# Optimization experiments

Measured on AMD Instinct MI355X. Metric: run time of the kernel, lower is better.

## Reference

```python
import jax, jax.numpy as jnp
import numpy as np

L, S, N, E, H = 1024, 1024, 4, 1024, 16


def setup_inputs() -> dict:
    key = jax.random.key(0)
    ks = jax.random.split(key, 7)
    return {
        "query": jax.random.normal(ks[0], (L, N, E), jnp.float32),
        "key": jax.random.normal(ks[1], (S, N, E), jnp.float32),
        "value": jax.random.normal(ks[2], (S, N, E), jnp.float32),
        "in_proj_weight": jax.random.normal(ks[3], (3 * E, E), jnp.float32) * (E ** -0.5),
        "in_proj_bias": jax.random.normal(ks[4], (3 * E,), jnp.float32) * 0.02,
        "out_proj_weight": jax.random.normal(ks[5], (E, E), jnp.float32) * (E ** -0.5),
        "out_proj_bias": jax.random.normal(ks[6], (E,), jnp.float32) * 0.02,
        "num_heads": H,
    }


def _split_heads(x, n, h, hd):
    # (T, N, E) -> (N*h, T, hd), matching torch view(T, N*h, hd).transpose(0, 1)
    t = x.shape[0]
    return jnp.transpose(x.reshape(t, n * h, hd), (1, 0, 2))


def reference(query, key, value, in_proj_weight, in_proj_bias,
              out_proj_weight, out_proj_bias, num_heads):
    tgt_len, bsz, embed_dim = query.shape
    src_len = key.shape[0]
    head_dim = embed_dim // num_heads
    scaling = float(head_dim) ** -0.5

    # packed QKV projection (torch F.linear: x @ W.T + b), sliced as in source
    q = query @ in_proj_weight[:embed_dim].T + in_proj_bias[:embed_dim]
    k = key @ in_proj_weight[embed_dim:2 * embed_dim].T + in_proj_bias[embed_dim:2 * embed_dim]
    v = value @ in_proj_weight[2 * embed_dim:].T + in_proj_bias[2 * embed_dim:]
    q = q * scaling

    q = _split_heads(q, bsz, num_heads, head_dim)  # (N*H, L, hd)
    k = _split_heads(k, bsz, num_heads, head_dim)  # (N*H, S, hd)
    v = _split_heads(v, bsz, num_heads, head_dim)  # (N*H, S, hd)

    scores = jnp.einsum('bld,bsd->bls', q, k)           # (N*H, L, S)
    attn = jax.nn.softmax(scores, axis=-1)
    ctx = jnp.einsum('bls,bsd->bld', attn, v)           # (N*H, L, hd)

    # (N*H, L, hd) -> (L, N, E)
    ctx = jnp.transpose(ctx, (1, 0, 2)).reshape(tgt_len, bsz, embed_dim)
    attn_output = ctx @ out_proj_weight.T + out_proj_bias

    # need_weights=True path: average over heads -> (N, L, S)
    attn_weights = attn.reshape(bsz, num_heads, tgt_len, src_len).sum(axis=1) / num_heads
    return attn_output, attn_weights
```

## Files before the change

### kernel.cpp

```cpp
#include <hip/hip_runtime.h>

typedef unsigned short u16;
typedef __attribute__((ext_vector_type(8))) short short8;
typedef __attribute__((ext_vector_type(4))) float f32x4;

__device__ __forceinline__ u16 f2bf(float f) {
  unsigned int i = __float_as_uint(f);
  i += 0x7fffu + ((i >> 16) & 1u);
  return (u16)(i >> 16);
}

__device__ __forceinline__ short8 cvt8(const float* p) {
  float4 a = ((const float4*)p)[0];
  float4 b = ((const float4*)p)[1];
  short8 r;
  r[0] = (short)f2bf(a.x); r[1] = (short)f2bf(a.y);
  r[2] = (short)f2bf(a.z); r[3] = (short)f2bf(a.w);
  r[4] = (short)f2bf(b.x); r[5] = (short)f2bf(b.y);
  r[6] = (short)f2bf(b.z); r[7] = (short)f2bf(b.w);
  return r;
}

__global__ __launch_bounds__(256) void convert_bf16(
    const float* __restrict__ q, const float* __restrict__ k,
    const float* __restrict__ v, const float* __restrict__ Wi,
    const float* __restrict__ Wo,
    u16* __restrict__ qb, u16* __restrict__ kb, u16* __restrict__ vb,
    u16* __restrict__ Wib, u16* __restrict__ Wob)
{
  const float* src; u16* dst; int len8;
  switch (blockIdx.y) {
    case 0:  src = q;  dst = qb;  len8 = 524288; break;
    case 1:  src = k;  dst = kb;  len8 = 524288; break;
    case 2:  src = v;  dst = vb;  len8 = 524288; break;
    case 3:  src = Wi; dst = Wib; len8 = 393216; break;
    default: src = Wo; dst = Wob; len8 = 131072; break;
  }
  int stride = gridDim.x * 256;
  for (int i = blockIdx.x * 256 + threadIdx.x; i < len8; i += stride)
    *(short8*)(dst + (size_t)i * 8) = cvt8(src + (size_t)i * 8);
}

__global__ __launch_bounds__(256) void qkv_gemm(
    const u16* __restrict__ qb, const u16* __restrict__ kb,
    const u16* __restrict__ vb, const u16* __restrict__ W,
    const float* __restrict__ bias,
    u16* __restrict__ qh, u16* __restrict__ kh, u16* __restrict__ vt)
{
  __shared__ __align__(16) u16 SH[24576];

  const int tid  = threadIdx.x;
  const int wave = tid >> 6;
  const int lane = tid & 63;
  const int r    = lane & 15;
  const int q4   = lane >> 4;
  const int wm   = wave >> 1;
  const int wn   = wave & 1;

  const int orig = blockIdx.y * 24 + blockIdx.x;
  const int nid  = (orig & 7) * 96 + (orig >> 3);
  const int mt   = nid / 24;
  const int jt   = nid - mt * 24;
  const int src  = jt >> 3;
  const u16* X = (src == 0) ? qb : (src == 1) ? kb : vb;
  const int m0 = mt * 128;
  const int j0 = jt * 128;

  const int lrow = lane >> 2;
  const int lchk = ((lane & 3) ^ ((lane >> 3) & 3)) << 4;
  const char* Xc = (const char*)X;
  const char* Wc = (const char*)W;
  const int fchk = (q4 ^ ((r >> 1) & 3)) << 3;

  f32x4 acc[4][4];
  #pragma unroll
  for (int a = 0; a < 4; ++a)
    #pragma unroll
    for (int b = 0; b < 4; ++b)
      acc[a][b] = (f32x4){0.f, 0.f, 0.f, 0.f};

  auto STAGE = [&](int buf, int kt) {
    const int kbyte = kt * 64;
    u16* Ad = SH + buf * 4096;
    u16* Bd = SH + 12288 + buf * 4096;
    #pragma unroll
    for (int i = 0; i < 2; ++i) {
      const int g = wave * 2 + i;
      __builtin_amdgcn_global_load_lds(
          (const u16*)(Xc + (size_t)(m0 + g * 16 + lrow) * 2048 + kbyte + lchk),
          Ad + g * 512, 16, 0, 0);
      __builtin_amdgcn_global_load_lds(
          (const u16*)(Wc + (size_t)(j0 + g * 16 + lrow) * 2048 + kbyte + lchk),
          Bd + g * 512, 16, 0, 0);
    }
  };

  auto COMPUTE = [&](int cb) {
    const u16* As = SH + cb * 4096;
    const u16* Bs = SH + 12288 + cb * 4096;
    short8 af[4], bf[4];
    #pragma unroll
    for (int mi = 0; mi < 4; ++mi)
      af[mi] = *(const short8*)(&As[(wm * 64 + mi * 16 + r) * 32 + fchk]);
    #pragma unroll
    for (int ji = 0; ji < 4; ++ji)
      bf[ji] = *(const short8*)(&Bs[(wn * 64 + ji * 16 + r) * 32 + fchk]);
    #pragma unroll
    for (int mi = 0; mi < 4; ++mi)
      #pragma unroll
      for (int ji = 0; ji < 4; ++ji)
        acc[mi][ji] = __builtin_amdgcn_mfma_f32_16x16x32_bf16(af[mi], bf[ji], acc[mi][ji], 0, 0, 0);
  };

  STAGE(0, 0);
  STAGE(1, 1);
  int cb = 0;
  for (int kt = 0; kt < 31; ++kt) {
    asm volatile("s_waitcnt vmcnt(4) lgkmcnt(0)\n\ts_barrier" ::: "memory");
    if (kt < 30) {
      int nb = cb + 2; if (nb >= 3) nb -= 3;
      STAGE(nb, kt + 2);
    }
    COMPUTE(cb);
    if (++cb == 3) cb = 0;
  }
  asm volatile("s_waitcnt vmcnt(0) lgkmcnt(0)\n\ts_barrier" ::: "memory");
  COMPUTE(cb);

  __syncthreads();
  const int h0 = (j0 & 1023) >> 6;
  const int t0 = mt * 32;
  if (src < 2) {
    #pragma unroll
    for (int mi = 0; mi < 4; ++mi) {
      const int tt = wm * 16 + mi * 4 + q4;
      #pragma unroll
      for (int ji = 0; ji < 4; ++ji) {
        const int jj = wn * 64 + ji * 16 + r;
        const int dd = jj & 63, hq = jj >> 6;
        const int cs = (((dd >> 3) ^ (tt & 7)) << 3) + (dd & 7);
        #pragma unroll
        for (int rr = 0; rr < 4; ++rr) {
          float v = acc[mi][ji][rr] + bias[j0 + jj];
          SH[((rr * 2 + hq) * 32 + tt) * 64 + cs] =
              (src == 0) ? f2bf(v * 0.125f) : f2bf(v);
        }
      }
    }
    __syncthreads();
    u16* dst = (src == 0) ? qh : kh;
    #pragma unroll
    for (int c = 0; c < 8; ++c) {
      const int cid = c * 256 + tid;
      const int nn = cid >> 9, hq = (cid >> 8) & 1, tt = (cid >> 3) & 31, dc = cid & 7;
      short8 vv = *(const short8*)(SH + ((nn * 2 + hq) * 32 + tt) * 64 +
                                   ((dc ^ (tt & 7)) << 3));
      *(short8*)(dst + (size_t)(nn * 16 + h0 + hq) * 65536 +
                 (size_t)(t0 + tt) * 64 + dc * 8) = vv;
    }
  } else {
    #pragma unroll
    for (int mi = 0; mi < 4; ++mi) {
      const int tt = wm * 16 + mi * 4 + q4;
      const int tc = tt >> 3, toff = tt & 7;
      #pragma unroll
      for (int ji = 0; ji < 4; ++ji) {
        const int jj = wn * 64 + ji * 16 + r;
        const int dd = jj & 63, hq = jj >> 6;
        #pragma unroll
        for (int rr = 0; rr < 4; ++rr) {
          float v = acc[mi][ji][rr] + bias[j0 + jj];
          SH[((rr * 2 + hq) * 64 + dd) * 32 + ((tc ^ (dd & 3)) << 3) + toff] = f2bf(v);
        }
      }
    }
    __syncthreads();
    #pragma unroll
    for (int c = 0; c < 8; ++c) {
      const int cid = c * 256 + tid;
      const int bbv = cid >> 8, dd = (cid >> 2) & 63, tc = cid & 3;
      short8 vv = *(const short8*)(SH + (bbv * 64 + dd) * 32 +
                                   ((tc ^ (dd & 3)) << 3));
      const int bb = (bbv >> 1) * 16 + h0 + (bbv & 1);
      *(short8*)(vt + (size_t)bb * 65536 + (size_t)dd * 1024 + t0 + tc * 8) = vv;
    }
  }
}

__global__ __launch_bounds__(512) void attn_ctx_mfma(
    const u16* __restrict__ qh, const u16* __restrict__ kh,
    const u16* __restrict__ vt, u16* __restrict__ ctx,
    float* __restrict__ Zbuf)
{
  __shared__ __align__(16) u16 Ks[2][4096];
  __shared__ __align__(16) u16 Vs[2][4096];
  __shared__ __align__(16) u16 Pl[8][1024];

  const int tid = threadIdx.x;
  const int wv = tid >> 6, lane = tid & 63, r = lane & 15, q4 = lane >> 4;
  const int b  = blockIdx.y;
  const int lw = blockIdx.x * 128 + wv * 16;
  const int n = b >> 4, h = b & 15;

  const u16* qbase = qh + (size_t)b * 65536;
  const char* kc = (const char*)(kh + (size_t)b * 65536);
  const char* vc = (const char*)(vt + (size_t)b * 65536);
  u16* P = Pl[wv];

  const int ls  = lane >> 3;
  const int swzb = ((lane & 7) ^ ls) << 4;
  const size_t klo = (size_t)wv * 1024  + (size_t)ls * 128  + swzb;
  const size_t vlo = (size_t)wv * 16384 + (size_t)ls * 2048 + swzb;

  const int rsw = r & 7;
  const int c0 = (q4 ^ rsw) << 3;
  const int c1 = ((q4 ^ rsw) ^ 4) << 3;

  short8 aq0 = *(const short8*)(qbase + (size_t)(lw + r) * 64 + q4 * 8);
  short8 aq1 = *(const short8*)(qbase + (size_t)(lw + r) * 64 + 32 + q4 * 8);

  f32x4 oc[4];
  #pragma unroll
  for (int ji = 0; ji < 4; ++ji) oc[ji] = (f32x4){0.f, 0.f, 0.f, 0.f};
  float z[4] = {0.f, 0.f, 0.f, 0.f};

  {
    __builtin_amdgcn_global_load_lds(kc + klo, &Ks[0][wv * 512], 16, 0, 0);
    __builtin_amdgcn_global_load_lds(vc + vlo, &Vs[0][wv * 512], 16, 0, 0);
  }

  for (int it = 0; it < 16; ++it) {
    const int cur = it & 1;
    __syncthreads();
    const u16* Kb = Ks[cur];
    const u16* Vb = Vs[cur];

    f32x4 sc[4];
    #pragma unroll
    for (int ji = 0; ji < 4; ++ji) {
      const int row = (ji * 16 + r) * 64;
      short8 bk0 = *(const short8*)(Kb + row + c0);
      short8 bk1 = *(const short8*)(Kb + row + c1);
      f32x4 t = (f32x4){0.f, 0.f, 0.f, 0.f};
      t = __builtin_amdgcn_mfma_f32_16x16x32_bf16(aq0, bk0, t, 0, 0, 0);
      t = __builtin_amdgcn_mfma_f32_16x16x32_bf16(aq1, bk1, t, 0, 0, 0);
      sc[ji] = t;
    }

    if (it < 15) {
      __builtin_amdgcn_global_load_lds(kc + (size_t)(it + 1) * 8192 + klo,
                                       &Ks[cur ^ 1][wv * 512], 16, 0, 0);
      __builtin_amdgcn_global_load_lds(vc + (size_t)(it + 1) * 128 + vlo,
                                       &Vs[cur ^ 1][wv * 512], 16, 0, 0);
    }

    #pragma unroll
    for (int ji = 0; ji < 4; ++ji) {
      const int cw = ji * 2 + (r >> 3);
      #pragma unroll
      for (int rr = 0; rr < 4; ++rr) {
        float e = __expf(sc[ji][rr]);
        z[rr] += e;
        const int row = q4 * 4 + rr;
        P[row * 64 + ((cw ^ (row & 7)) << 3) + (r & 7)] = f2bf(e);
      }
    }
    asm volatile("s_waitcnt lgkmcnt(0)" ::: "memory");
    short8 ap0 = *(const short8*)(P + r * 64 + c0);
    short8 ap1 = *(const short8*)(P + r * 64 + c1);
    #pragma unroll
    for (int ji = 0; ji < 4; ++ji) {
      const int row = (ji * 16 + r) * 64;
      short8 bv0 = *(const short8*)(Vb + row + c0);
      short8 bv1 = *(const short8*)(Vb + row + c1);
      oc[ji] = __builtin_amdgcn_mfma_f32_16x16x32_bf16(ap0, bv0, oc[ji], 0, 0, 0);
      oc[ji] = __builtin_amdgcn_mfma_f32_16x16x32_bf16(ap1, bv1, oc[ji], 0, 0, 0);
    }
  }

  #pragma unroll
  for (int rr = 0; rr < 4; ++rr) {
    float zz = z[rr];
    zz += __shfl_xor(zz, 1);
    zz += __shfl_xor(zz, 2);
    zz += __shfl_xor(zz, 4);
    zz += __shfl_xor(zz, 8);
    z[rr] = zz;
  }

  #pragma unroll
  for (int rr = 0; rr < 4; ++rr) {
    float inv = 1.0f / z[rr];
    int l = lw + q4 * 4 + rr;
    u16* crow = ctx + ((size_t)l * 4 + n) * 1024 + h * 64;
    #pragma unroll
    for (int ji = 0; ji < 4; ++ji)
      crow[ji * 16 + r] = f2bf(oc[ji][rr] * inv);
    if (r == 0) Zbuf[(size_t)b * 1024 + l] = z[rr];
  }
}

__global__ __launch_bounds__(256) void tail_fused(
    const u16* __restrict__ qh, const u16* __restrict__ kh,
    const float* __restrict__ Zbuf, float* __restrict__ out_w,
    const u16* __restrict__ ctx, const u16* __restrict__ W,
    const float* __restrict__ bias, float* __restrict__ out)
{
  __shared__ __align__(16) u16 SH[18432];

  const int tid = threadIdx.x;
  const int wv = tid >> 6, lane = tid & 63, r = lane & 15, q4 = lane >> 4;

  if (blockIdx.x < 512) {
    const int wave = wv;
    const int wm   = wave >> 1;
    const int wn   = wave & 1;
    const int orig = blockIdx.x;
    const int nid  = (orig & 7) * 64 + (orig >> 3);
    const int mt   = nid >> 4;
    const int jt   = nid & 15;
    const int m0 = mt * 128;
    const int j0 = jt * 64;

    const int lrow = lane >> 2;
    const int lchk = ((lane & 3) ^ ((lane >> 3) & 3)) << 4;
    const char* Ac = (const char*)ctx;
    const char* Wc = (const char*)W;
    const int fchk = (q4 ^ ((r >> 1) & 3)) << 3;

    f32x4 acc[4][2];
    #pragma unroll
    for (int a = 0; a < 4; ++a)
      #pragma unroll
      for (int b = 0; b < 2; ++b)
        acc[a][b] = (f32x4){0.f, 0.f, 0.f, 0.f};

    auto STAGE = [&](int buf, int kt) {
      const int kbyte = kt * 64;
      u16* Ad = SH + buf * 4096;
      u16* Bd = SH + 12288 + buf * 2048;
      #pragma unroll
      for (int i = 0; i < 2; ++i) {
        const int g = wave * 2 + i;
        __builtin_amdgcn_global_load_lds(
            (const u16*)(Ac + (size_t)(m0 + g * 16 + lrow) * 2048 + kbyte + lchk),
            Ad + g * 512, 16, 0, 0);
      }
      __builtin_amdgcn_global_load_lds(
          (const u16*)(Wc + (size_t)(j0 + wave * 16 + lrow) * 2048 + kbyte + lchk),
          Bd + wave * 512, 16, 0, 0);
    };

    auto COMPUTE = [&](int cb) {
      const u16* As = SH + cb * 4096;
      const u16* Bs = SH + 12288 + cb * 2048;
      short8 af[4], bf[2];
      #pragma unroll
      for (int mi = 0; mi < 4; ++mi)
        af[mi] = *(const short8*)(&As[(wm * 64 + mi * 16 + r) * 32 + fchk]);
      #pragma unroll
      for (int ji = 0; ji < 2; ++ji)
        bf[ji] = *(const short8*)(&Bs[(wn * 32 + ji * 16 + r) * 32 + fchk]);
      #pragma unroll
      for (int mi = 0; mi < 4; ++mi)
        #pragma unroll
        for (int ji = 0; ji < 2; ++ji)
          acc[mi][ji] = __builtin_amdgcn_mfma_f32_16x16x32_bf16(af[mi], bf[ji], acc[mi][ji], 0, 0, 0);
    };

    STAGE(0, 0);
    STAGE(1, 1);
    int cb = 0;
    for (int kt = 0; kt < 31; ++kt) {
      asm volatile("s_waitcnt vmcnt(3) lgkmcnt(0)\n\ts_barrier" ::: "memory");
      if (kt < 30) {
        int nb = cb + 2; if (nb >= 3) nb -= 3;
        STAGE(nb, kt + 2);
      }
      COMPUTE(cb);
      if (++cb == 3) cb = 0;
    }
    asm volatile("s_waitcnt vmcnt(0) lgkmcnt(0)\n\ts_barrier" ::: "memory");
    COMPUTE(cb);

    #pragma unroll
    for (int mi = 0; mi < 4; ++mi) {
      #pragma unroll
      for (int ji = 0; ji < 2; ++ji) {
        #pragma unroll
        for (int rr = 0; rr < 4; ++rr) {
          int m = m0 + wm * 64 + mi * 16 + q4 * 4 + rr;
          int j = j0 + wn * 32 + ji * 16 + r;
          out[(size_t)m * 1024 + j] = acc[mi][ji][rr] + bias[j];
        }
      }
    }
  } else {
    const int id2 = blockIdx.x - 512;
    const int lt = id2 & 15;
    const int st = (id2 >> 4) & 15;
    const int n  = id2 >> 8;
    const int l0 = lt * 64;
    const int s0 = st * 64;
    const int lw = l0 + wv * 16;

    u16* Kw = SH;
    float* invZ = (float*)(SH + 12288);

    const char* khc = (const char*)kh + (size_t)n * 2097152;

    const int ls  = lane >> 3;
    const int swzb = ((lane & 7) ^ ls) << 4;
    const int iw  = wv * 2;
    const size_t klo = (size_t)s0 * 128 + (size_t)iw * 1024 + (size_t)ls * 128 + swzb;

    const int rsw = r & 7;
    const int c0 = (q4 ^ rsw) << 3;
    const int c1 = ((q4 ^ rsw) ^ 4) << 3;

    for (int i = tid; i < 1024; i += 256) {
      int hh = i >> 6, row = i & 63;
      invZ[hh * 64 + row] = 1.0f / (Zbuf[(size_t)(n * 16 + hh) * 1024 + l0 + row] * 16.0f);
    }

    auto STAGEK = [&](int buf, int hh) {
      const char* kp = khc + (size_t)hh * 131072 + klo;
      u16* kd = &Kw[buf * 4096 + iw * 512];
      __builtin_amdgcn_global_load_lds(kp,        kd,       16, 0, 0);
      __builtin_amdgcn_global_load_lds(kp + 1024, kd + 512, 16, 0, 0);
    };

    STAGEK(0, 0);
    STAGEK(1, 1);
    const u16* q0 = qh + (size_t)(n * 16) * 65536;
    short8 aqc0 = *(const short8*)(q0 + (size_t)(lw + r) * 64 + q4 * 8);
    short8 aqc1 = *(const short8*)(q0 + (size_t)(lw + r) * 64 + 32 + q4 * 8);

    f32x4 wacc[4];
    #pragma unroll
    for (int ji = 0; ji < 4; ++ji) wacc[ji] = (f32x4){0.f, 0.f, 0.f, 0.f};

    auto HEAD = [&](int hh, int cbw, short8& an0, short8& an1) {
      const int hn = (hh < 15) ? hh + 1 : hh;
      const u16* qn = qh + (size_t)(n * 16 + hn) * 65536;
      an0 = *(const short8*)(qn + (size_t)(lw + r) * 64 + q4 * 8);
      an1 = *(const short8*)(qn + (size_t)(lw + r) * 64 + 32 + q4 * 8);
      if (hh < 14) {
        int nb = cbw + 2; if (nb >= 3) nb -= 3;
        STAGEK(nb, hh + 2);
      }
      const u16* Kb = Kw + cbw * 4096;
      f32x4 sc[4];
      #pragma unroll
      for (int ji = 0; ji < 4; ++ji) {
        const int row = (ji * 16 + r) * 64;
        short8 bk0 = *(const short8*)(Kb + row + c0);
        short8 bk1 = *(const short8*)(Kb + row + c1);
        f32x4 t = (f32x4){0.f, 0.f, 0.f, 0.f};
        t = __builtin_amdgcn_mfma_f32_16x16x32_bf16(aqc0, bk0, t, 0, 0, 0);
        t = __builtin_amdgcn_mfma_f32_16x16x32_bf16(aqc1, bk1, t, 0, 0, 0);
        sc[ji] = t;
      }
      #pragma unroll
      for (int rr = 0; rr < 4; ++rr) {
        float iv = invZ[hh * 64 + wv * 16 + q4 * 4 + rr];
        #pragma unroll
        for (int ji = 0; ji < 4; ++ji)
          wacc[ji][rr] += __expf(sc[ji][rr]) * iv;
      }
      aqc0 = an0; aqc1 = an1;
    };

    int cbw = 0;
    short8 an0, an1;
    for (int hh = 0; hh < 15; ++hh) {
      asm volatile("s_waitcnt vmcnt(4) lgkmcnt(0)\n\ts_barrier" ::: "memory");
      HEAD(hh, cbw, an0, an1);
      if (++cbw == 3) cbw = 0;
    }
    asm volatile("s_waitcnt vmcnt(0) lgkmcnt(0)\n\ts_barrier" ::: "memory");
    HEAD(15, cbw, an0, an1);

    #pragma unroll
    for (int ji = 0; ji < 4; ++ji)
      #pragma unroll
      for (int rr = 0; rr < 4; ++rr) {
        int row = lw + q4 * 4 + rr;
        int col = s0 + ji * 16 + r;
        out_w[(size_t)n * 1048576 + (size_t)row * 1024 + col] = wacc[ji][rr];
      }
  }
}

extern "C" void kernel_launch(void* const* d_in, const int* in_sizes, int n_in,
                              void* d_out, int out_size, void* d_ws, size_t ws_size,
                              hipStream_t stream) {
  const float* query = (const float*)d_in[0];
  const float* key   = (const float*)d_in[1];
  const float* value = (const float*)d_in[2];
  const float* W_in  = (const float*)d_in[3];
  const float* b_in  = (const float*)d_in[4];
  const float* W_out = (const float*)d_in[5];
  const float* b_out = (const float*)d_in[6];
  float* out = (float*)d_out;

  u16* qb  = (u16*)d_ws;
  u16* kb  = qb  + (size_t)4194304;
  u16* vb  = kb  + (size_t)4194304;
  u16* Wib = vb  + (size_t)4194304;
  u16* Wob = Wib + (size_t)3145728;
  u16* qh  = Wob + (size_t)1048576;
  u16* kh  = qh  + (size_t)4194304;
  u16* vt  = kh  + (size_t)4194304;
  u16* ctx = vt  + (size_t)4194304;
  float* Zbuf = (float*)(ctx + (size_t)4194304);

  convert_bf16<<<dim3(512, 5), 256, 0, stream>>>(query, key, value, W_in, W_out,
                                                 qb, kb, vb, Wib, Wob);
  qkv_gemm<<<dim3(24, 32), 256, 0, stream>>>(qb, kb, vb, Wib, b_in, qh, kh, vt);
  attn_ctx_mfma<<<dim3(8, 64), 512, 0, stream>>>(qh, kh, vt, ctx, Zbuf);
  tail_fused<<<dim3(1536), 256, 0, stream>>>(qh, kh, Zbuf, out + (size_t)4194304,
                                             ctx, Wob, b_out, out);
}
```

Baseline: 215.1 us.

## Fuse fp32-to-bf16 conversion into QKV GEMM with register-staged double buffering

Removes the separate convert_bf16 kernel and has the QKV GEMM load fp32 inputs and weights directly from global memory into registers, convert them to bf16, and write them to swizzled LDS. The output-projection weight conversion is folded into the start of the GEMM blocks. The pipeline changes from a 3-stage async global_load_lds scheme to 2-stage register prefetch with __syncthreads. This avoids a kernel launch and a bf16 write/read round trip, but doubles the global bytes read per tile and re-converts the operands in every block that reuses them.

```diff
diff --git a/kernel.cpp b/kernel.cpp
--- a/kernel.cpp
+++ b/kernel.cpp
@@ -10,9 +10,7 @@
   return (u16)(i >> 16);
 }
 
-__device__ __forceinline__ short8 cvt8(const float* p) {
-  float4 a = ((const float4*)p)[0];
-  float4 b = ((const float4*)p)[1];
+__device__ __forceinline__ short8 pack8(float4 a, float4 b) {
   short8 r;
   r[0] = (short)f2bf(a.x); r[1] = (short)f2bf(a.y);
   r[2] = (short)f2bf(a.z); r[3] = (short)f2bf(a.w);
@@ -21,33 +19,14 @@
   return r;
 }
 
-__global__ __launch_bounds__(256) void convert_bf16(
-    const float* __restrict__ q, const float* __restrict__ k,
-    const float* __restrict__ v, const float* __restrict__ Wi,
-    const float* __restrict__ Wo,
-    u16* __restrict__ qb, u16* __restrict__ kb, u16* __restrict__ vb,
-    u16* __restrict__ Wib, u16* __restrict__ Wob)
+__global__ __launch_bounds__(256) void qkv_gemm(
+    const float* __restrict__ qf, const float* __restrict__ kf,
+    const float* __restrict__ vf, const float* __restrict__ Wf,
+    const float* __restrict__ Wof, const float* __restrict__ bias,
+    u16* __restrict__ qh, u16* __restrict__ kh, u16* __restrict__ vt,
+    u16* __restrict__ Wob)
 {
-  const float* src; u16* dst; int len8;
-  switch (blockIdx.y) {
-    case 0:  src = q;  dst = qb;  len8 = 524288; break;
-    case 1:  src = k;  dst = kb;  len8 = 524288; break;
-    case 2:  src = v;  dst = vb;  len8 = 524288; break;
-    case 3:  src = Wi; dst = Wib; len8 = 393216; break;
-    default: src = Wo; dst = Wob; len8 = 131072; break;
-  }
-  int stride = gridDim.x * 256;
-  for (int i = blockIdx.x * 256 + threadIdx.x; i < len8; i += stride)
-    *(short8*)(dst + (size_t)i * 8) = cvt8(src + (size_t)i * 8);
-}
-
-__global__ __launch_bounds__(256) void qkv_gemm(
-    const u16* __restrict__ qb, const u16* __restrict__ kb,
-    const u16* __restrict__ vb, const u16* __restrict__ W,
-    const float* __restrict__ bias,
-    u16* __restrict__ qh, u16* __restrict__ kh, u16* __restrict__ vt)
-{
-  __shared__ __align__(16) u16 SH[24576];
+  __shared__ __align__(16) u16 SH[16384];
 
   const int tid  = threadIdx.x;
   const int wave = tid >> 6;
@@ -58,18 +37,27 @@
   const int wn   = wave & 1;
 
   const int orig = blockIdx.y * 24 + blockIdx.x;
+
+  {
+    const int gtid = orig * 256 + tid;
+    if (gtid < 131072) {
+      float4 a = ((const float4*)Wof)[gtid * 2];
+      float4 b = ((const float4*)Wof)[gtid * 2 + 1];
+      *(short8*)(Wob + (size_t)gtid * 8) = pack8(a, b);
+    }
+  }
+
   const int nid  = (orig & 7) * 96 + (orig >> 3);
   const int mt   = nid / 24;
   const int jt   = nid - mt * 24;
   const int src  = jt >> 3;
-  const u16* X = (src == 0) ? qb : (src == 1) ? kb : vb;
+  const float* Xf = (src == 0) ? qf : (src == 1) ? kf : vf;
   const int m0 = mt * 128;
   const int j0 = jt * 128;
 
   const int lrow = lane >> 2;
-  const int lchk = ((lane & 3) ^ ((lane >> 3) & 3)) << 4;
-  const char* Xc = (const char*)X;
-  const char* Wc = (const char*)W;
+  const int lch  = lane & 3;
+  const int wchk = (lch ^ ((lane >> 3) & 3)) << 3;
   const int fchk = (q4 ^ ((r >> 1) & 3)) << 3;
 
   f32x4 acc[4][4];
@@ -79,25 +67,37 @@
     for (int b = 0; b < 4; ++b)
       acc[a][b] = (f32x4){0.f, 0.f, 0.f, 0.f};
 
-  auto STAGE = [&](int buf, int kt) {
-    const int kbyte = kt * 64;
-    u16* Ad = SH + buf * 4096;
-    u16* Bd = SH + 12288 + buf * 4096;
+  float4 ra[4], rb[4];
+
+  auto LOADR = [&](int kt) {
+    const size_t fo = (size_t)kt * 32 + lch * 8;
     #pragma unroll
     for (int i = 0; i < 2; ++i) {
       const int g = wave * 2 + i;
-      __builtin_amdgcn_global_load_lds(
-          (const u16*)(Xc + (size_t)(m0 + g * 16 + lrow) * 2048 + kbyte + lchk),
-          Ad + g * 512, 16, 0, 0);
-      __builtin_amdgcn_global_load_lds(
-          (const u16*)(Wc + (size_t)(j0 + g * 16 + lrow) * 2048 + kbyte + lchk),
-          Bd + g * 512, 16, 0, 0);
+      const float* pa = Xf + (size_t)(m0 + g * 16 + lrow) * 1024 + fo;
+      const float* pb = Wf + (size_t)(j0 + g * 16 + lrow) * 1024 + fo;
+      ra[i * 2]     = *(const float4*)(pa);
+      ra[i * 2 + 1] = *(const float4*)(pa + 4);
+      rb[i * 2]     = *(const float4*)(pb);
+      rb[i * 2 + 1] = *(const float4*)(pb + 4);
+    }
+  };
+
+  auto WRITER = [&](int buf) {
+    u16* Ad = SH + buf * 4096;
+    u16* Bd = SH + 8192 + buf * 4096;
+    #pragma unroll
+    for (int i = 0; i < 2; ++i) {
+      const int g = wave * 2 + i;
+      const int ro = (g * 16 + lrow) * 32 + wchk;
+      *(short8*)(Ad + ro) = pack8(ra[i * 2], ra[i * 2 + 1]);
+      *(short8*)(Bd + ro) = pack8(rb[i * 2], rb[i * 2 + 1]);
     }
   };
 
   auto COMPUTE = [&](int cb) {
     const u16* As = SH + cb * 4096;
-    const u16* Bs = SH + 12288 + cb * 4096;
+    const u16* Bs = SH + 8192 + cb * 4096;
     short8 af[4], bf[4];
     #pragma unroll
     for (int mi = 0; mi < 4; ++mi)
@@ -112,20 +112,17 @@
         acc[mi][ji] = __builtin_amdgcn_mfma_f32_16x16x32_bf16(af[mi], bf[ji], acc[mi][ji], 0, 0, 0);
   };
 
-  STAGE(0, 0);
-  STAGE(1, 1);
-  int cb = 0;
-  for (int kt = 0; kt < 31; ++kt) {
-    asm volatile("s_waitcnt vmcnt(4) lgkmcnt(0)\n\ts_barrier" ::: "memory");
-    if (kt < 30) {
-      int nb = cb + 2; if (nb >= 3) nb -= 3;
-      STAGE(nb, kt + 2);
-    }
-    COMPUTE(cb);
-    if (++cb == 3) cb = 0;
-  }
-  asm volatile("s_waitcnt vmcnt(0) lgkmcnt(0)\n\ts_barrier" ::: "memory");
-  COMPUTE(cb);
+  LOADR(0);
+  WRITER(0);
+  LOADR(1);
+
+  for (int kt = 0; kt < 32; ++kt) {
+    const int cur = kt & 1;
+    __syncthreads();
+    if (kt < 31) WRITER(cur ^ 1);
+    if (kt < 30) LOADR(kt + 2);
+    COMPUTE(cur);
+  }
 
   __syncthreads();
   const int h0 = (j0 & 1023) >> 6;
@@ -514,10 +511,10 @@
   u16* vt  = kh  + (size_t)4194304;
   u16* ctx = vt  + (size_t)4194304;
   float* Zbuf = (float*)(ctx + (size_t)4194304);
-
-  convert_bf16<<<dim3(512, 5), 256, 0, stream>>>(query, key, value, W_in, W_out,
-                                                 qb, kb, vb, Wib, Wob);
-  qkv_gemm<<<dim3(24, 32), 256, 0, stream>>>(qb, kb, vb, Wib, b_in, qh, kh, vt);
+  (void)qb; (void)kb; (void)vb;
+
+  qkv_gemm<<<dim3(24, 32), 256, 0, stream>>>(query, key, value, W_in, W_out,
+                                             b_in, qh, kh, vt, Wob);
   attn_ctx_mfma<<<dim3(8, 64), 512, 0, stream>>>(qh, kh, vt, ctx, Zbuf);
   tail_fused<<<dim3(1536), 256, 0, stream>>>(qh, kh, Zbuf, out + (size_t)4194304,
                                              ctx, Wob, b_out, out);
```

Measured after the change: 247.3 us. 1.15x slower.
